# Performance work log

Hardware: AMD Instinct MI355X
Metric: run time of the kernel (lower is better)

The kernel has to match this reference:

```python
import jax, jax.numpy as jnp
import numpy as np

NUM_NODE_TYPES = 4
NUM_EDGE_TYPES = 12
OUT_SHAPE = (3, 3)


def setup_inputs() -> dict:
    key = jax.random.key(0)
    k1, k2, k3, k4, k5 = jax.random.split(key, 5)
    N, E, C = 100000, 1600000, 64
    in_dim = C * 2 + NUM_NODE_TYPES * 2 + NUM_EDGE_TYPES  # 148
    out_dim = int(np.prod(OUT_SHAPE))  # 9
    return {
        "x": jax.random.normal(k1, (N, C), dtype=jnp.float32),
        "edge_index": jax.random.randint(k2, (2, E), 0, N, dtype=jnp.int64),
        "edge_types": jax.random.randint(k3, (E,), 0, NUM_EDGE_TYPES, dtype=jnp.int64),
        "node_types": jax.random.randint(k4, (N,), 0, NUM_NODE_TYPES, dtype=jnp.int64),
        "W": jax.random.normal(k5, (out_dim, in_dim), dtype=jnp.float32) * 0.08,
    }


def reference(x, edge_index, edge_types, node_types, W):
    src, dst = edge_index[0], edge_index[1]
    x_src = x[src]                      # [E, C]
    x_dst = x[dst]                      # [E, C]
    nt_oh = jax.nn.one_hot(node_types, NUM_NODE_TYPES, dtype=x.dtype)  # [N, 4]
    src_type = nt_oh[src]               # [E, 4]
    dst_type = nt_oh[dst]               # [E, 4]
    edge_type = jax.nn.one_hot(edge_types, NUM_EDGE_TYPES, dtype=x.dtype)  # [E, 12]
    x_cat = jnp.concatenate([x_src, x_dst, src_type, dst_type, edge_type], axis=1)  # [E, 148]
    maps = x_cat @ W.T                  # [E, 9], bias-free linear
    maps = jnp.tanh(maps)
    return maps.reshape(-1, OUT_SHAPE[0], OUT_SHAPE[1])
```

## Files before the change

kernel.cpp:

```cpp
#include <hip/hip_runtime.h>
#include <math.h>

#define C 64
#define IN_DIM 148
#define ODIM 9
#define EPT 2
#define BE (256 * EPT)

typedef _Float16 half_t;
typedef float f4 __attribute__((ext_vector_type(4)));
typedef _Float16 h2 __attribute__((ext_vector_type(2)));
typedef unsigned int u32;
typedef u32 u4 __attribute__((ext_vector_type(4)));
typedef int i2 __attribute__((ext_vector_type(2)));

__device__ __forceinline__ float tanh_fast(float x) {
    float e = __expf(2.0f * x);
    return 1.0f - 2.0f / (e + 1.0f);
}

__device__ __forceinline__ void decode9(u4 w, int u[ODIM]) {
    u[0] = w.x & 0xFFF;
    u[1] = (w.x >> 12) & 0xFFF;
    u[2] = __builtin_amdgcn_alignbit(w.y, w.x, 24) & 0xFFF;
    u[3] = (w.y >> 4) & 0xFFF;
    u[4] = (w.y >> 16) & 0xFFF;
    u[5] = __builtin_amdgcn_alignbit(w.z, w.y, 28) & 0xFFF;
    u[6] = (w.z >> 8) & 0xFFF;
    u[7] = (w.z >> 20) & 0xFFF;
    u[8] = w.w & 0xFFF;
}

__global__ __launch_bounds__(256) void node_proj_kernel(
    const float* __restrict__ x, const int* __restrict__ node_types,
    const float* __restrict__ W, u4* __restrict__ sp, u4* __restrict__ dp,
    int N)
{
    __shared__ _Float16 Wh[2 * ODIM][C];
    __shared__ float ntab[2][ODIM][4];

    for (int i = threadIdx.x; i < 2 * ODIM * C; i += 256) {
        int r = i >> 6, c = i & 63;
        int o = (r < ODIM) ? r : r - ODIM;
        int col = (r < ODIM) ? c : (C + c);
        Wh[r][c] = (_Float16)W[o * IN_DIM + col];
    }
    for (int i = threadIdx.x; i < 2 * ODIM * 4; i += 256) {
        int t = i & 3;
        int o = (i >> 2) % ODIM;
        int sd = (i >> 2) / ODIM;
        ntab[sd][o][t] = W[o * IN_DIM + 128 + sd * 4 + t];
    }
    __syncthreads();

    int tid = blockIdx.x * 256 + threadIdx.x;
    int n = tid >> 1;
    int h = tid & 1;
    if (n >= N) return;

    const f4* xr = (const f4*)(x + (size_t)n * C);
    h2 xh[32];
#pragma unroll
    for (int q = 0; q < 16; ++q) {
        f4 v = xr[q];
        xh[2 * q]     = h2{(_Float16)v.x, (_Float16)v.y};
        xh[2 * q + 1] = h2{(_Float16)v.z, (_Float16)v.w};
    }

    float acc[ODIM];
#pragma unroll
    for (int o = 0; o < ODIM; ++o) acc[o] = 0.0f;

#pragma unroll
    for (int g = 0; g < 8; ++g) {
#pragma unroll
        for (int o = 0; o < ODIM; ++o) {
            const h2* wp = (const h2*)&Wh[h * ODIM + o][g * 8];
            acc[o] = __builtin_amdgcn_fdot2(xh[4 * g + 0], wp[0], acc[o], false);
            acc[o] = __builtin_amdgcn_fdot2(xh[4 * g + 1], wp[1], acc[o], false);
            acc[o] = __builtin_amdgcn_fdot2(xh[4 * g + 2], wp[2], acc[o], false);
            acc[o] = __builtin_amdgcn_fdot2(xh[4 * g + 3], wp[3], acc[o], false);
        }
    }

    int t = node_types[n];
    u32 u[ODIM];
#pragma unroll
    for (int o = 0; o < ODIM; ++o) {
        float v = acc[o] + ntab[h][o][t];
        int q = (int)rintf(fmaf(v, 256.0f, 2048.0f));
        q = q < 0 ? 0 : (q > 4095 ? 4095 : q);
        u[o] = (u32)q;
    }
    u4 w;
    w.x = u[0] | (u[1] << 12) | (u[2] << 24);
    w.y = (u[2] >> 8) | (u[3] << 4) | (u[4] << 16) | (u[5] << 28);
    w.z = (u[5] >> 4) | (u[6] << 8) | (u[7] << 20);
    w.w = u[8];

    (h ? dp : sp)[n] = w;
}

__global__ __launch_bounds__(256) void edge_kernel(
    const int* __restrict__ ei, const int* __restrict__ etypes,
    const u4* __restrict__ sp, const u4* __restrict__ dp,
    const float* __restrict__ W, float* __restrict__ out,
    int E)
{
    __shared__ float etab2[12][ODIM];
    __shared__ alignas(16) float sm[BE * ODIM];

    for (int i = threadIdx.x; i < 12 * ODIM; i += 256) {
        int t = i / ODIM, o = i - t * ODIM;
        etab2[t][o] = W[o * IN_DIM + 136 + t] - 16.0f;
    }
    __syncthreads();

    int base = blockIdx.x * BE;
    int e0 = base + threadIdx.x * EPT;

    i2 s2, d2, t2;
    if (e0 + EPT <= E) {
        s2 = __builtin_nontemporal_load((const i2*)(ei + e0));
        d2 = __builtin_nontemporal_load((const i2*)(ei + (size_t)E + e0));
        t2 = __builtin_nontemporal_load((const i2*)(etypes + e0));
    } else {
#pragma unroll
        for (int k = 0; k < EPT; ++k) {
            int e = e0 + k; if (e > E - 1) e = E - 1;
            s2[k] = ei[e]; d2[k] = ei[(size_t)E + e]; t2[k] = etypes[e];
        }
    }

    u4 sw[EPT], dw[EPT];
#pragma unroll
    for (int k = 0; k < EPT; ++k) sw[k] = sp[s2[k]];
#pragma unroll
    for (int k = 0; k < EPT; ++k) dw[k] = dp[d2[k]];

#pragma unroll
    for (int k = 0; k < EPT; ++k) {
        int us[ODIM], ud[ODIM];
        decode9(sw[k], us);
        decode9(dw[k], ud);
        const float* eb = &etab2[t2[k]][0];
        float* smrow = &sm[(threadIdx.x * EPT + k) * ODIM];
#pragma unroll
        for (int o = 0; o < ODIM; ++o) {
            float v = fmaf((float)(us[o] + ud[o]), 1.0f / 256.0f, eb[o]);
            smrow[o] = tanh_fast(v);
        }
    }
    __syncthreads();

    float* ob = out + (size_t)base * ODIM;
    int cnt = E - base; if (cnt > BE) cnt = BE;
    if (cnt == BE) {
        const f4* smv = (const f4*)sm;
        f4* obv = (f4*)ob;
#pragma unroll
        for (int j = threadIdx.x; j < BE * ODIM / 4; j += 256)
            __builtin_nontemporal_store(smv[j], obv + j);
    } else {
        int tot = cnt * ODIM;
        for (int j = threadIdx.x; j < tot; j += 256)
            __builtin_nontemporal_store(sm[j], ob + j);
    }
}

extern "C" void kernel_launch(void* const* d_in, const int* in_sizes, int n_in,
                              void* d_out, int out_size, void* d_ws, size_t ws_size,
                              hipStream_t stream) {
    const float* x      = (const float*)d_in[0];
    const int*   ei     = (const int*)d_in[1];
    const int*   etypes = (const int*)d_in[2];
    const int*   ntypes = (const int*)d_in[3];
    const float* W      = (const float*)d_in[4];
    float* out = (float*)d_out;

    int N = in_sizes[0] / C;
    int E = in_sizes[2];

    u4* sp = (u4*)d_ws;
    u4* dp = sp + N;

    int nthreads = N * 2;
    int nblocks  = (nthreads + 255) / 256;
    node_proj_kernel<<<nblocks, 256, 0, stream>>>(x, ntypes, W, sp, dp, N);

    int eblocks = (E + BE - 1) / BE;
    edge_kernel<<<eblocks, 256, 0, stream>>>(ei, etypes, sp, dp, W, out, E);
}
```

Measured before the change: 45.85 us.

## Split each edge's gather across a quad of lanes with DPP neighbor exchange

The edge kernel now assigns a quad of four lanes to a group of four edges. Each lane gathers one 32-bit word of the packed 16-byte source and destination projections instead of one lane loading the whole 16 bytes. Lanes exchange adjacent words via DPP so each can decode three of the nine 12-bit outputs and compute their tanh. Blocks shrink to 256 edges. The aim is more memory requests in flight and less per-thread decode work, at the cost of four times as many narrow gather instructions, one idle output slot per quad, and twice as many blocks.

Result: no change. 45.30 us (-1.2%).

```diff
diff --git a/kernel.cpp b/kernel.cpp
--- a/kernel.cpp
+++ b/kernel.cpp
@@ -4,31 +4,24 @@
 #define C 64
 #define IN_DIM 148
 #define ODIM 9
-#define EPT 2
-#define BE (256 * EPT)
+#define QEDGES 4
+#define BE 256
 
 typedef _Float16 half_t;
 typedef float f4 __attribute__((ext_vector_type(4)));
 typedef _Float16 h2 __attribute__((ext_vector_type(2)));
 typedef unsigned int u32;
+typedef unsigned long long u64;
 typedef u32 u4 __attribute__((ext_vector_type(4)));
-typedef int i2 __attribute__((ext_vector_type(2)));
+typedef int i4 __attribute__((ext_vector_type(4)));
 
 __device__ __forceinline__ float tanh_fast(float x) {
     float e = __expf(2.0f * x);
     return 1.0f - 2.0f / (e + 1.0f);
 }
 
-__device__ __forceinline__ void decode9(u4 w, int u[ODIM]) {
-    u[0] = w.x & 0xFFF;
-    u[1] = (w.x >> 12) & 0xFFF;
-    u[2] = __builtin_amdgcn_alignbit(w.y, w.x, 24) & 0xFFF;
-    u[3] = (w.y >> 4) & 0xFFF;
-    u[4] = (w.y >> 16) & 0xFFF;
-    u[5] = __builtin_amdgcn_alignbit(w.z, w.y, 28) & 0xFFF;
-    u[6] = (w.z >> 8) & 0xFFF;
-    u[7] = (w.z >> 20) & 0xFFF;
-    u[8] = w.w & 0xFFF;
+__device__ __forceinline__ u32 quad_down1(u32 v) {
+    return (u32)__builtin_amdgcn_mov_dpp((int)v, 0xF9, 0xF, 0xF, true);
 }
 
 __global__ __launch_bounds__(256) void node_proj_kernel(
@@ -103,7 +96,7 @@
 
 __global__ __launch_bounds__(256) void edge_kernel(
     const int* __restrict__ ei, const int* __restrict__ etypes,
-    const u4* __restrict__ sp, const u4* __restrict__ dp,
+    const u32* __restrict__ sp, const u32* __restrict__ dp,
     const float* __restrict__ W, float* __restrict__ out,
     int E)
 {
@@ -117,38 +110,47 @@
     __syncthreads();
 
     int base = blockIdx.x * BE;
-    int e0 = base + threadIdx.x * EPT;
+    int quad = threadIdx.x >> 2;
+    int sub  = threadIdx.x & 3;
+    int e0 = base + quad * QEDGES;
 
-    i2 s2, d2, t2;
-    if (e0 + EPT <= E) {
-        s2 = __builtin_nontemporal_load((const i2*)(ei + e0));
-        d2 = __builtin_nontemporal_load((const i2*)(ei + (size_t)E + e0));
-        t2 = __builtin_nontemporal_load((const i2*)(etypes + e0));
+    i4 s4, d4, t4;
+    if (e0 + QEDGES <= E) {
+        s4 = __builtin_nontemporal_load((const i4*)(ei + e0));
+        d4 = __builtin_nontemporal_load((const i4*)(ei + (size_t)E + e0));
+        t4 = __builtin_nontemporal_load((const i4*)(etypes + e0));
     } else {
 #pragma unroll
-        for (int k = 0; k < EPT; ++k) {
+        for (int k = 0; k < QEDGES; ++k) {
             int e = e0 + k; if (e > E - 1) e = E - 1;
-            s2[k] = ei[e]; d2[k] = ei[(size_t)E + e]; t2[k] = etypes[e];
+            s4[k] = ei[e]; d4[k] = ei[(size_t)E + e]; t4[k] = etypes[e];
         }
     }
 
-    u4 sw[EPT], dw[EPT];
+    u32 ws[QEDGES], wd[QEDGES];
 #pragma unroll
-    for (int k = 0; k < EPT; ++k) sw[k] = sp[s2[k]];
+    for (int k = 0; k < QEDGES; ++k) ws[k] = sp[(size_t)s4[k] * 4 + sub];
 #pragma unroll
-    for (int k = 0; k < EPT; ++k) dw[k] = dp[d2[k]];
+    for (int k = 0; k < QEDGES; ++k) wd[k] = dp[(size_t)d4[k] * 4 + sub];
 
+    int off0 = sub * 4;
 #pragma unroll
-    for (int k = 0; k < EPT; ++k) {
-        int us[ODIM], ud[ODIM];
-        decode9(sw[k], us);
-        decode9(dw[k], ud);
-        const float* eb = &etab2[t2[k]][0];
-        float* smrow = &sm[(threadIdx.x * EPT + k) * ODIM];
+    for (int k = 0; k < QEDGES; ++k) {
+        u32 nbs = quad_down1(ws[k]);
+        u32 nbd = quad_down1(wd[k]);
+        u64 WS = ((u64)nbs << 32) | ws[k];
+        u64 WD = ((u64)nbd << 32) | wd[k];
+        int el = quad * QEDGES + k;
+        const float* eb = &etab2[t4[k]][0];
 #pragma unroll
-        for (int o = 0; o < ODIM; ++o) {
-            float v = fmaf((float)(us[o] + ud[o]), 1.0f / 256.0f, eb[o]);
-            smrow[o] = tanh_fast(v);
+        for (int j = 0; j < 3; ++j) {
+            int o = 3 * sub + j;
+            int oc = o < ODIM ? o : ODIM - 1;
+            u32 us = (u32)(WS >> (off0 + 12 * j)) & 0xFFF;
+            u32 ud = (u32)(WD >> (off0 + 12 * j)) & 0xFFF;
+            float v = fmaf((float)(us + ud), 1.0f / 256.0f, eb[oc]);
+            float r = tanh_fast(v);
+            if (o < ODIM) sm[el * ODIM + o] = r;
         }
     }
     __syncthreads();
@@ -189,5 +191,6 @@
     node_proj_kernel<<<nblocks, 256, 0, stream>>>(x, ntypes, W, sp, dp, N);
 
     int eblocks = (E + BE - 1) / BE;
-    edge_kernel<<<eblocks, 256, 0, stream>>>(ei, etypes, sp, dp, W, out, E);
+    edge_kernel<<<eblocks, 256, 0, stream>>>(ei, etypes, (const u32*)sp, (const u32*)dp,
+                                             W, out, E);
 }
```
